# Kernel tuning notes

Hardware: AMD Instinct MI355X
Metric: run time of the kernel (lower is better)

The kernel has to match this reference:

```python
import jax, jax.numpy as jnp
import numpy as np

N_NODES = 100_000
N_EDGES = 1_250_000
IN_CH = 64
HID = 64
OUT_CH = 10
K = 5
NUM_GRAPHS = 64


def setup_inputs() -> dict:
    key = jax.random.key(0)
    ks = jax.random.split(key, 8)
    x = jax.random.normal(ks[0], (N_NODES, IN_CH), dtype=jnp.float32)
    edge_index = jax.random.randint(ks[1], (2, N_EDGES), 0, N_NODES)
    batch = jnp.sort(jax.random.randint(ks[2], (N_NODES,), 0, NUM_GRAPHS))
    s_in = float(1.0 / np.sqrt(IN_CH))
    s_h = float(1.0 / np.sqrt(HID))
    W1 = jax.random.uniform(ks[3], (K, IN_CH, HID), minval=-s_in, maxval=s_in, dtype=jnp.float32)
    b1 = jnp.zeros((HID,), jnp.float32)
    W2 = jax.random.uniform(ks[4], (K, HID, HID), minval=-s_h, maxval=s_h, dtype=jnp.float32)
    b2 = jnp.zeros((HID,), jnp.float32)
    Wfc = jax.random.uniform(ks[5], (HID, OUT_CH), minval=-s_h, maxval=s_h, dtype=jnp.float32)
    bfc = jnp.zeros((OUT_CH,), jnp.float32)
    return dict(x=x, edge_index=edge_index, batch=batch,
                W1=W1, b1=b1, W2=W2, b2=b2, Wfc=Wfc, bfc=bfc)


def _cheb_conv(x, src, dst, W, b):
    """PyG ChebConv with normalization='rw', lambda_max=2.
    L_rw = I - D^{-1} A ; scaled L_hat = 2*L/lambda_max - I = -D^{-1}A
    (self-loop weights cancel to 0), so each hop is a weighted scatter-add."""
    n = x.shape[0]
    deg = jax.ops.segment_sum(jnp.ones((src.shape[0],), x.dtype), src, num_segments=n)
    inv_deg = jnp.where(deg > 0, 1.0 / deg, 0.0)
    ew = -inv_deg[src]  # per-edge weight of L_hat

    def prop(t):  # (L_hat t)[i] = sum_{j->i} ew * t[j]
        return jax.ops.segment_sum(ew[:, None] * t[src], dst, num_segments=n)

    Tx0 = x
    out = Tx0 @ W[0]
    Tx1 = prop(Tx0)
    out = out + Tx1 @ W[1]
    for k in range(2, W.shape[0]):
        Tx2 = 2.0 * prop(Tx1) - Tx0
        out = out + Tx2 @ W[k]
        Tx0, Tx1 = Tx1, Tx2
    return out + b


def reference(x, edge_index, batch, W1, b1, W2, b2, Wfc, bfc):
    src, dst = edge_index[0], edge_index[1]
    h = jax.nn.selu(_cheb_conv(x, src, dst, W1, b1))
    # AlphaDropout is identity at inference
    h = jax.nn.selu(_cheb_conv(h, src, dst, W2, b2))
    g = jax.ops.segment_sum(h, batch, num_segments=NUM_GRAPHS)  # global_add_pool
    return g @ Wfc + bfc
```

## Files before the change

kernel.cpp:

```cpp
#include <hip/hip_runtime.h>
#include <cstdint>

#define CH 64
#define NBLK 256
#define NBMAX 1024
#define SRCMASK 0x1FFFFu

typedef __attribute__((ext_vector_type(8))) short bf16x8;
typedef __attribute__((ext_vector_type(8))) unsigned short u16x8;
typedef __attribute__((ext_vector_type(4))) float f32x4;
typedef unsigned int uint32;
typedef unsigned char uchar;

__device__ __forceinline__ unsigned short f2bf(float x) {
  unsigned u = __float_as_uint(x);
  u += 0x7FFF + ((u >> 16) & 1);
  return (unsigned short)(u >> 16);
}
__device__ __forceinline__ float bflo(uint32 u) { return __uint_as_float(u << 16); }
__device__ __forceinline__ float bfhi(uint32 u) { return __uint_as_float(u & 0xFFFF0000u); }
__device__ __forceinline__ uint32 bfpack(float lo, float hi) {
  return ((uint32)f2bf(hi) << 16) | (uint32)f2bf(lo);
}

__global__ __launch_bounds__(256) void k_b1(const int* __restrict__ src, const int* __restrict__ dst,
                                            int* __restrict__ cntD, int* __restrict__ cntS, int E, int NB) {
  __shared__ int hD[NBMAX], hS[NBMAX];
  int t = threadIdx.x, b = blockIdx.x;
  for (int i = t; i < NBMAX; i += 256) { hD[i] = 0; hS[i] = 0; }
  __syncthreads();
  int chunk = (E + NBLK - 1) / NBLK;
  int e0 = b * chunk, e1 = min(E, e0 + chunk);
  for (int e = e0 + t; e < e1; e += 256) {
    atomicAdd(&hD[dst[e] >> 7], 1);
    atomicAdd(&hS[src[e] >> 7], 1);
  }
  __syncthreads();
  for (int i = t; i < NB; i += 256) {
    cntD[i * NBLK + b] = hD[i];
    cntS[i * NBLK + b] = hS[i];
  }
}

__global__ __launch_bounds__(256) void k_scan_local(const int* __restrict__ in, int* __restrict__ out,
                                                    int* __restrict__ bsum, int total) {
  __shared__ int s[256];
  int t = threadIdx.x;
  int base = blockIdx.x * 1024 + t * 4;
  int v0 = (base + 0 < total) ? in[base + 0] : 0;
  int v1 = (base + 1 < total) ? in[base + 1] : 0;
  int v2 = (base + 2 < total) ? in[base + 2] : 0;
  int v3 = (base + 3 < total) ? in[base + 3] : 0;
  int sum = v0 + v1 + v2 + v3;
  s[t] = sum;
  __syncthreads();
  for (int off = 1; off < 256; off <<= 1) {
    int x = (t >= off) ? s[t - off] : 0;
    __syncthreads();
    s[t] += x;
    __syncthreads();
  }
  int excl = s[t] - sum;
  if (base + 0 < total) out[base + 0] = excl;  excl += v0;
  if (base + 1 < total) out[base + 1] = excl;  excl += v1;
  if (base + 2 < total) out[base + 2] = excl;  excl += v2;
  if (base + 3 < total) out[base + 3] = excl;
  if (t == 255) bsum[blockIdx.x] = s[255];
}

__global__ __launch_bounds__(256) void k_scan_bsums(int* bsum, int nb) {
  __shared__ int s[256];
  int t = threadIdx.x;
  int v = (t < nb) ? bsum[t] : 0;
  s[t] = v;
  __syncthreads();
  for (int off = 1; off < 256; off <<= 1) {
    int x = (t >= off) ? s[t - off] : 0;
    __syncthreads();
    s[t] += x;
    __syncthreads();
  }
  if (t < nb) bsum[t] = s[t] - v;
}

__global__ __launch_bounds__(256) void k_scan_add(int* __restrict__ arr, const int* __restrict__ bsum, int total) {
  int i = blockIdx.x * 256 + threadIdx.x;
  if (i < total) arr[i] += bsum[i >> 10];
}

__global__ __launch_bounds__(256) void k_b2(const int* __restrict__ src, const int* __restrict__ dst,
                                            const int* __restrict__ cbaseD, const int* __restrict__ cbaseS,
                                            uint32* __restrict__ etmp, uchar* __restrict__ svals, int E, int NB) {
  __shared__ int curD[NBMAX], curS[NBMAX];
  int t = threadIdx.x, b = blockIdx.x;
  for (int i = t; i < NB; i += 256) {
    curD[i] = cbaseD[i * NBLK + b];
    curS[i] = cbaseS[i * NBLK + b];
  }
  __syncthreads();
  int chunk = (E + NBLK - 1) / NBLK;
  int e0 = b * chunk, e1 = min(E, e0 + chunk);
  for (int e = e0 + t; e < e1; e += 256) {
    int s = src[e], d = dst[e];
    int pd = atomicAdd(&curD[d >> 7], 1);
    etmp[pd] = ((uint32)(d & 127) << 17) | (uint32)s;
    int ps = atomicAdd(&curS[s >> 7], 1);
    svals[ps] = (uchar)(s & 127);
  }
}

__global__ __launch_bounds__(256) void k_b3_deg(const uchar* __restrict__ svals, const int* __restrict__ cbaseS,
                                                float* __restrict__ neg_inv, int n, int E, int NB) {
  __shared__ int h[128];
  int t = threadIdx.x, k = blockIdx.x;
  if (t < 128) h[t] = 0;
  __syncthreads();
  int lo = cbaseS[k * NBLK];
  int hi = (k + 1 < NB) ? cbaseS[(k + 1) * NBLK] : E;
  for (int e = lo + t; e < hi; e += 256) atomicAdd(&h[svals[e]], 1);
  __syncthreads();
  if (t < 128) {
    int node = k * 128 + t;
    if (node < n) {
      int c = h[t];
      neg_inv[node] = c > 0 ? (-1.0f / (float)c) : 0.0f;
    }
  }
}

__global__ __launch_bounds__(256) void k_b3_dst(const uint32* __restrict__ etmp, const int* __restrict__ cbaseD,
                                                const float* __restrict__ neg_inv, int2* __restrict__ erec,
                                                int* __restrict__ row_ptr, int n, int E, int NB) {
  __shared__ int h[128], sc[128], cur[128];
  int t = threadIdx.x, k = blockIdx.x;
  if (t < 128) h[t] = 0;
  __syncthreads();
  int lo = cbaseD[k * NBLK];
  int hi = (k + 1 < NB) ? cbaseD[(k + 1) * NBLK] : E;
  for (int e = lo + t; e < hi; e += 256) atomicAdd(&h[(etmp[e] >> 17) & 127], 1);
  __syncthreads();
  if (t < 128) sc[t] = h[t];
  __syncthreads();
  for (int off = 1; off < 128; off <<= 1) {
    int x = (t < 128 && t >= off) ? sc[t - off] : 0;
    __syncthreads();
    if (t < 128) sc[t] += x;
    __syncthreads();
  }
  if (t < 128) {
    int excl = sc[t] - h[t];
    cur[t] = excl;
    int node = k * 128 + t;
    if (node < n) row_ptr[node] = lo + excl;
  }
  if (k == NB - 1 && t == 0) row_ptr[n] = E;
  __syncthreads();
  for (int e = lo + t; e < hi; e += 256) {
    uint32 r = etmp[e];
    int s = (int)(r & SRCMASK);
    int pos = atomicAdd(&cur[(r >> 17) & 127], 1);
    erec[lo + pos] = make_int2(s, __float_as_int(neg_inv[s]));
  }
}

__global__ __launch_bounds__(256) void k_cast(const float* __restrict__ x, unsigned short* __restrict__ xb,
                                              int total8) {
  int i = blockIdx.x * 256 + threadIdx.x;
  if (i < total8) {
    const float4* p = (const float4*)(x + (size_t)i * 8);
    float4 v0 = p[0], v1 = p[1];
    u16x8 w;
    w[0] = f2bf(v0.x); w[1] = f2bf(v0.y); w[2] = f2bf(v0.z); w[3] = f2bf(v0.w);
    w[4] = f2bf(v1.x); w[5] = f2bf(v1.y); w[6] = f2bf(v1.z); w[7] = f2bf(v1.w);
    *(u16x8*)(xb + (size_t)i * 8) = w;
  }
}

__global__ __launch_bounds__(256) void k_prop(const int* __restrict__ row_ptr, const int2* __restrict__ erec,
                                              const uint32* __restrict__ t_in,
                                              const uint32* __restrict__ t_sub,
                                              uint32* __restrict__ t_out, int n, int mode) {
  int tid = threadIdx.x;
  int lane = tid & 63;
  int cp = lane & 31;
  int h = lane >> 5;
  int node = blockIdx.x * 8 + ((tid >> 6) << 1) + h;
  bool active = node < n;
  int beg = active ? row_ptr[node] : 0;
  int end = active ? row_ptr[node + 1] : 0;
  float a0 = 0.f, a1 = 0.f, b0 = 0.f, b1 = 0.f, c0 = 0.f, c1 = 0.f, d0 = 0.f, d1 = 0.f;
  float e0a = 0.f, e1a = 0.f, f0 = 0.f, f1 = 0.f, g0 = 0.f, g1 = 0.f, h0 = 0.f, h1 = 0.f;
  int e = beg;
  for (; e + 8 <= end; e += 8) {
    int2 q0 = erec[e + 0]; int2 q1 = erec[e + 1]; int2 q2 = erec[e + 2]; int2 q3 = erec[e + 3];
    int2 q4 = erec[e + 4]; int2 q5 = erec[e + 5]; int2 q6 = erec[e + 6]; int2 q7 = erec[e + 7];
    uint32 u0 = t_in[q0.x * 32 + cp];
    uint32 u1 = t_in[q1.x * 32 + cp];
    uint32 u2 = t_in[q2.x * 32 + cp];
    uint32 u3 = t_in[q3.x * 32 + cp];
    uint32 u4 = t_in[q4.x * 32 + cp];
    uint32 u5 = t_in[q5.x * 32 + cp];
    uint32 u6 = t_in[q6.x * 32 + cp];
    uint32 u7 = t_in[q7.x * 32 + cp];
    float w0 = __int_as_float(q0.y), w1 = __int_as_float(q1.y);
    float w2 = __int_as_float(q2.y), w3 = __int_as_float(q3.y);
    float w4 = __int_as_float(q4.y), w5 = __int_as_float(q5.y);
    float w6 = __int_as_float(q6.y), w7 = __int_as_float(q7.y);
    a0 = fmaf(w0, bflo(u0), a0);   a1 = fmaf(w0, bfhi(u0), a1);
    b0 = fmaf(w1, bflo(u1), b0);   b1 = fmaf(w1, bfhi(u1), b1);
    c0 = fmaf(w2, bflo(u2), c0);   c1 = fmaf(w2, bfhi(u2), c1);
    d0 = fmaf(w3, bflo(u3), d0);   d1 = fmaf(w3, bfhi(u3), d1);
    e0a = fmaf(w4, bflo(u4), e0a); e1a = fmaf(w4, bfhi(u4), e1a);
    f0 = fmaf(w5, bflo(u5), f0);   f1 = fmaf(w5, bfhi(u5), f1);
    g0 = fmaf(w6, bflo(u6), g0);   g1 = fmaf(w6, bfhi(u6), g1);
    h0 = fmaf(w7, bflo(u7), h0);   h1 = fmaf(w7, bfhi(u7), h1);
  }
  if (e + 4 <= end) {
    int2 q0 = erec[e + 0]; int2 q1 = erec[e + 1]; int2 q2 = erec[e + 2]; int2 q3 = erec[e + 3];
    uint32 u0 = t_in[q0.x * 32 + cp];
    uint32 u1 = t_in[q1.x * 32 + cp];
    uint32 u2 = t_in[q2.x * 32 + cp];
    uint32 u3 = t_in[q3.x * 32 + cp];
    float w0 = __int_as_float(q0.y), w1 = __int_as_float(q1.y);
    float w2 = __int_as_float(q2.y), w3 = __int_as_float(q3.y);
    a0 = fmaf(w0, bflo(u0), a0);   a1 = fmaf(w0, bfhi(u0), a1);
    b0 = fmaf(w1, bflo(u1), b0);   b1 = fmaf(w1, bfhi(u1), b1);
    c0 = fmaf(w2, bflo(u2), c0);   c1 = fmaf(w2, bfhi(u2), c1);
    d0 = fmaf(w3, bflo(u3), d0);   d1 = fmaf(w3, bfhi(u3), d1);
    e += 4;
  }
  if (e + 2 <= end) {
    int2 q0 = erec[e + 0]; int2 q1 = erec[e + 1];
    uint32 u0 = t_in[q0.x * 32 + cp];
    uint32 u1 = t_in[q1.x * 32 + cp];
    float w0 = __int_as_float(q0.y), w1 = __int_as_float(q1.y);
    a0 = fmaf(w0, bflo(u0), a0);   a1 = fmaf(w0, bfhi(u0), a1);
    b0 = fmaf(w1, bflo(u1), b0);   b1 = fmaf(w1, bfhi(u1), b1);
    e += 2;
  }
  if (e < end) {
    int2 q = erec[e];
    uint32 u = t_in[q.x * 32 + cp];
    float w = __int_as_float(q.y);
    a0 = fmaf(w, bflo(u), a0);
    a1 = fmaf(w, bfhi(u), a1);
  }
  float s0 = ((a0 + b0) + (c0 + d0)) + ((e0a + f0) + (g0 + h0));
  float s1 = ((a1 + b1) + (c1 + d1)) + ((e1a + f1) + (g1 + h1));
  if (active) {
    if (mode == 2) {
      uint32 u = t_sub[(size_t)node * 32 + cp];
      s0 = 2.0f * s0 - bflo(u);
      s1 = 2.0f * s1 - bfhi(u);
    }
    t_out[(size_t)node * 32 + cp] = bfpack(s0, s1);
  }
}

__global__ __launch_bounds__(256) void k_prepW(const float* __restrict__ W, unsigned short* __restrict__ Wt) {
  int o = blockIdx.x * 256 + threadIdx.x;
  if (o < 64 * 320) {
    int j = o / 320, k = o - j * 320;
    Wt[o] = f2bf(W[k * 64 + j]);
  }
}

__device__ __forceinline__ float selu(float v) {
  const float sc = 1.0507009873554805f, al = 1.6732632423543773f;
  return (v > 0.f) ? (sc * v) : (sc * al * (expf(v) - 1.f));
}

__global__ __launch_bounds__(256) void k_gemm5(
    const unsigned short* __restrict__ M0, const unsigned short* __restrict__ M1,
    const unsigned short* __restrict__ M2, const unsigned short* __restrict__ M3,
    const unsigned short* __restrict__ M4,
    const unsigned short* __restrict__ Wt, const float* __restrict__ bias,
    unsigned short* __restrict__ outp, int n, int nstrips) {
  __shared__ unsigned short lds[2][32 * 320];
  const int t = threadIdx.x;
  const int lane = t & 63, wave = t >> 6;
  const int g = lane >> 4, r16 = lane & 15;
  const unsigned short* mats[5] = {M0, M1, M2, M3, M4};
  const int colB = wave * 16 + r16;
  bf16x8 Bf[10];
#pragma unroll
  for (int kk = 0; kk < 10; ++kk)
    Bf[kk] = *(const bf16x8*)(Wt + colB * 320 + kk * 32 + g * 8);
  const float bv = bias[colB];
  const int srow = t >> 3, scc = t & 7;

  int strip = blockIdx.x;
  if (strip >= nstrips) return;
  int cur = 0;
  {
    int node0 = strip * 32;
#pragma unroll
    for (int m = 0; m < 5; ++m) {
      int ca = m * 8 + scc;
      u16x8 w = {};
      if (node0 + srow < n)
        w = *(const u16x8*)(mats[m] + (size_t)(node0 + srow) * CH + scc * 8);
      *(u16x8*)(&lds[0][srow * 320 + ((ca ^ (srow & 7)) << 3)]) = w;
    }
  }
  __syncthreads();
  for (; strip < nstrips; strip += gridDim.x) {
    int nxt = strip + gridDim.x;
    if (nxt < nstrips) {
      int node0 = nxt * 32;
#pragma unroll
      for (int m = 0; m < 5; ++m) {
        int ca = m * 8 + scc;
        u16x8 w = {};
        if (node0 + srow < n)
          w = *(const u16x8*)(mats[m] + (size_t)(node0 + srow) * CH + scc * 8);
        *(u16x8*)(&lds[cur ^ 1][srow * 320 + ((ca ^ (srow & 7)) << 3)]) = w;
      }
    }
    const unsigned short* L = lds[cur];
    const int rowA0 = r16, rowA1 = r16 + 16;
    f32x4 acc0 = {}, acc1 = {};
#pragma unroll
    for (int kk = 0; kk < 10; ++kk) {
      int ca = kk * 4 + g;
      bf16x8 a0 = *(const bf16x8*)(&L[rowA0 * 320 + ((ca ^ (rowA0 & 7)) << 3)]);
      bf16x8 a1 = *(const bf16x8*)(&L[rowA1 * 320 + ((ca ^ (rowA1 & 7)) << 3)]);
      acc0 = __builtin_amdgcn_mfma_f32_16x16x32_bf16(a0, Bf[kk], acc0, 0, 0, 0);
      acc1 = __builtin_amdgcn_mfma_f32_16x16x32_bf16(a1, Bf[kk], acc1, 0, 0, 0);
    }
    int node0 = strip * 32;
    const f32x4 accs[2] = {acc0, acc1};
#pragma unroll
    for (int i = 0; i < 2; ++i) {
#pragma unroll
      for (int rr = 0; rr < 4; ++rr) {
        int row = node0 + i * 16 + g * 4 + rr;
        if (row < n)
          outp[(size_t)row * CH + colB] = f2bf(selu(accs[i][rr] + bv));
      }
    }
    __syncthreads();
    cur ^= 1;
  }
}

__global__ __launch_bounds__(256) void k_gemm5_pool(
    const unsigned short* __restrict__ M0, const unsigned short* __restrict__ M1,
    const unsigned short* __restrict__ M2, const unsigned short* __restrict__ M3,
    const unsigned short* __restrict__ M4,
    const unsigned short* __restrict__ Wt, const float* __restrict__ bias,
    const int* __restrict__ batch, float* __restrict__ gout, int n, int nstrips) {
  __shared__ unsigned short lds[2][32 * 320];
  const int t = threadIdx.x;
  const int lane = t & 63, wave = t >> 6;
  const int g = lane >> 4, r16 = lane & 15;
  const unsigned short* mats[5] = {M0, M1, M2, M3, M4};
  const int colB = wave * 16 + r16;
  bf16x8 Bf[10];
#pragma unroll
  for (int kk = 0; kk < 10; ++kk)
    Bf[kk] = *(const bf16x8*)(Wt + colB * 320 + kk * 32 + g * 8);
  const float bv = bias[colB];
  const int srow = t >> 3, scc = t & 7;

  int strip = blockIdx.x;
  if (strip >= nstrips) return;
  int cur = 0;
  {
    int node0 = strip * 32;
#pragma unroll
    for (int m = 0; m < 5; ++m) {
      int ca = m * 8 + scc;
      u16x8 w = {};
      if (node0 + srow < n)
        w = *(const u16x8*)(mats[m] + (size_t)(node0 + srow) * CH + scc * 8);
      *(u16x8*)(&lds[0][srow * 320 + ((ca ^ (srow & 7)) << 3)]) = w;
    }
  }
  __syncthreads();
  for (; strip < nstrips; strip += gridDim.x) {
    int nxt = strip + gridDim.x;
    if (nxt < nstrips) {
      int node0 = nxt * 32;
#pragma unroll
      for (int m = 0; m < 5; ++m) {
        int ca = m * 8 + scc;
        u16x8 w = {};
        if (node0 + srow < n)
          w = *(const u16x8*)(mats[m] + (size_t)(node0 + srow) * CH + scc * 8);
        *(u16x8*)(&lds[cur ^ 1][srow * 320 + ((ca ^ (srow & 7)) << 3)]) = w;
      }
    }
    const unsigned short* L = lds[cur];
    const int rowA0 = r16, rowA1 = r16 + 16;
    f32x4 acc0 = {}, acc1 = {};
#pragma unroll
    for (int kk = 0; kk < 10; ++kk) {
      int ca = kk * 4 + g;
      bf16x8 a0 = *(const bf16x8*)(&L[rowA0 * 320 + ((ca ^ (rowA0 & 7)) << 3)]);
      bf16x8 a1 = *(const bf16x8*)(&L[rowA1 * 320 + ((ca ^ (rowA1 & 7)) << 3)]);
      acc0 = __builtin_amdgcn_mfma_f32_16x16x32_bf16(a0, Bf[kk], acc0, 0, 0, 0);
      acc1 = __builtin_amdgcn_mfma_f32_16x16x32_bf16(a1, Bf[kk], acc1, 0, 0, 0);
    }
    __syncthreads();
    float* S = (float*)lds[cur];
    const f32x4 accs[2] = {acc0, acc1};
#pragma unroll
    for (int i = 0; i < 2; ++i)
#pragma unroll
      for (int rr = 0; rr < 4; ++rr) {
        int row = i * 16 + g * 4 + rr;
        S[row * 65 + colB] = selu(accs[i][rr] + bv);
      }
    __syncthreads();
    int node0 = strip * 32;
    int c = t & 63, w = t >> 6;
    float curv = 0.f;
    int curg = -1;
    for (int r = 0; r < 8; ++r) {
      int row = w * 8 + r;
      int gn = node0 + row;
      if (gn >= n) break;
      int b = batch[gn];
      if (b != curg) {
        if (curg >= 0) atomicAdd(&gout[curg * CH + c], curv);
        curg = b;
        curv = 0.f;
      }
      curv += S[row * 65 + c];
    }
    if (curg >= 0) atomicAdd(&gout[curg * CH + c], curv);
    __syncthreads();
    cur ^= 1;
  }
}

__global__ __launch_bounds__(256) void k_fc(const float* __restrict__ g, const float* __restrict__ Wfc,
                                            const float* __restrict__ bfc, float* __restrict__ outp,
                                            int ng, int oc) {
  int i = blockIdx.x * 256 + threadIdx.x;
  if (i < ng * oc) {
    int gi = i / oc, o = i - gi * oc;
    float s = bfc[o];
    for (int ci = 0; ci < CH; ++ci) s += g[gi * CH + ci] * Wfc[ci * oc + o];
    outp[i] = s;
  }
}

extern "C" void kernel_launch(void* const* d_in, const int* in_sizes, int n_in,
                              void* d_out, int out_size, void* d_ws, size_t ws_size,
                              hipStream_t stream) {
  const float* x   = (const float*)d_in[0];
  const int* eidx  = (const int*)d_in[1];
  const int* batch = (const int*)d_in[2];
  const float* W1  = (const float*)d_in[3];
  const float* b1  = (const float*)d_in[4];
  const float* W2  = (const float*)d_in[5];
  const float* b2  = (const float*)d_in[6];
  const float* Wfc = (const float*)d_in[7];
  const float* bfc = (const float*)d_in[8];
  float* out = (float*)d_out;

  const int n  = in_sizes[0] / CH;
  const int E  = in_sizes[1] / 2;
  const int OC = in_sizes[8];
  const int NG = out_size / OC;
  const int NB = (n + 127) >> 7;

  const int* src = eidx;
  const int* dst = eidx + E;

  size_t off = 0;
  char* base = (char*)d_ws;
  auto alloc = [&](size_t bytes) -> void* {
    size_t cur = (off + 255) & ~(size_t)255;
    off = cur + bytes;
    return (void*)(base + cur);
  };
  const int scan_total = NB * NBLK;
  const int scan_nb    = (scan_total + 1023) / 1024;
  int*   cntD   = (int*)alloc((size_t)scan_total * 4);
  int*   cntS   = (int*)alloc((size_t)scan_total * 4);
  int*   bsumD  = (int*)alloc((size_t)scan_nb * 4);
  int*   bsumS  = (int*)alloc((size_t)scan_nb * 4);
  float* neg_inv = (float*)alloc((size_t)n * 4);
  int*   row_ptr = (int*)alloc((size_t)(n + 1) * 4);
  int2*  erec    = (int2*)alloc((size_t)E * 8);
  const size_t tb16 = (size_t)n * CH * 2;
  unsigned short* Xb = (unsigned short*)alloc(tb16);
  unsigned short* T1 = (unsigned short*)alloc(tb16);
  unsigned short* T2 = (unsigned short*)alloc(tb16);
  unsigned short* T3 = (unsigned short*)alloc(tb16);
  unsigned short* T4 = (unsigned short*)alloc(tb16);
  unsigned short* H  = (unsigned short*)alloc(tb16);
  uint32* etmp  = (uint32*)alloc((size_t)E * 4);
  uchar*  svals = (uchar*)alloc((size_t)E);
  float* g  = (float*)alloc((size_t)NG * CH * 4);
  unsigned short* Wt1 = (unsigned short*)alloc(64 * 320 * 2);
  unsigned short* Wt2 = (unsigned short*)alloc(64 * 320 * 2);
  if (off > ws_size) return;

  hipMemsetAsync(g, 0, (size_t)NG * CH * 4, stream);

  k_b1<<<NBLK, 256, 0, stream>>>(src, dst, cntD, cntS, E, NB);
  k_scan_local<<<scan_nb, 256, 0, stream>>>(cntD, cntD, bsumD, scan_total);
  k_scan_bsums<<<1, 256, 0, stream>>>(bsumD, scan_nb);
  k_scan_add<<<(scan_total + 255) / 256, 256, 0, stream>>>(cntD, bsumD, scan_total);
  k_scan_local<<<scan_nb, 256, 0, stream>>>(cntS, cntS, bsumS, scan_total);
  k_scan_bsums<<<1, 256, 0, stream>>>(bsumS, scan_nb);
  k_scan_add<<<(scan_total + 255) / 256, 256, 0, stream>>>(cntS, bsumS, scan_total);
  k_b2<<<NBLK, 256, 0, stream>>>(src, dst, cntD, cntS, etmp, svals, E, NB);
  k_b3_deg<<<NB, 256, 0, stream>>>(svals, cntS, neg_inv, n, E, NB);
  k_b3_dst<<<NB, 256, 0, stream>>>(etmp, cntD, neg_inv, erec, row_ptr, n, E, NB);

  k_prepW<<<80, 256, 0, stream>>>(W1, Wt1);
  k_prepW<<<80, 256, 0, stream>>>(W2, Wt2);
  k_cast<<<(n * CH / 8 + 255) / 256, 256, 0, stream>>>(x, Xb, n * CH / 8);

  const int pb = (n + 7) / 8;
  const int nstrips = (n + 31) / 32;
  const int gb = nstrips < 1024 ? nstrips : 1024;
  k_prop<<<pb, 256, 0, stream>>>(row_ptr, erec, (const uint32*)Xb, nullptr, (uint32*)T1, n, 1);
  k_prop<<<pb, 256, 0, stream>>>(row_ptr, erec, (const uint32*)T1, (const uint32*)Xb, (uint32*)T2, n, 2);
  k_prop<<<pb, 256, 0, stream>>>(row_ptr, erec, (const uint32*)T2, (const uint32*)T1, (uint32*)T3, n, 2);
  k_prop<<<pb, 256, 0, stream>>>(row_ptr, erec, (const uint32*)T3, (const uint32*)T2, (uint32*)T4, n, 2);
  k_gemm5<<<gb, 256, 0, stream>>>(Xb, T1, T2, T3, T4, Wt1, b1, H, n, nstrips);
  k_prop<<<pb, 256, 0, stream>>>(row_ptr, erec, (const uint32*)H,  nullptr, (uint32*)T1, n, 1);
  k_prop<<<pb, 256, 0, stream>>>(row_ptr, erec, (const uint32*)T1, (const uint32*)H,  (uint32*)T2, n, 2);
  k_prop<<<pb, 256, 0, stream>>>(row_ptr, erec, (const uint32*)T2, (const uint32*)T1, (uint32*)T3, n, 2);
  k_prop<<<pb, 256, 0, stream>>>(row_ptr, erec, (const uint32*)T3, (const uint32*)T2, (uint32*)T4, n, 2);
  k_gemm5_pool<<<gb, 256, 0, stream>>>(H, T1, T2, T3, T4, Wt2, b2, batch, g, n, nstrips);
  k_fc<<<(NG * OC + 255) / 256, 256, 0, stream>>>(g, Wfc, bfc, out, NG, OC);
}
```

Baseline: 398.7 us.

## Fold Chebyshev recurrence into weights, merge scans, vectorize edge loads

Propagation kernels now compute plain powers of L_hat, with no 2*prop - T_{k-2} step. The Chebyshev polynomial coefficients are folded into the prepared GEMM weights, so the extra read of a previous tensor per hop goes away. The two count scans are merged into one scan over a concatenated buffer, with the S offsets shifted by E. Edge records are read as 16-byte pairs after aligning to an even index. Using monomial powers in bf16 can lose precision, since coefficients up to 8 amplify rounding.

```diff
diff --git a/kernel.cpp b/kernel.cpp
--- a/kernel.cpp
+++ b/kernel.cpp
@@ -46,12 +46,14 @@
                                                     int* __restrict__ bsum, int total) {
   __shared__ int s[256];
   int t = threadIdx.x;
-  int base = blockIdx.x * 1024 + t * 4;
-  int v0 = (base + 0 < total) ? in[base + 0] : 0;
-  int v1 = (base + 1 < total) ? in[base + 1] : 0;
-  int v2 = (base + 2 < total) ? in[base + 2] : 0;
-  int v3 = (base + 3 < total) ? in[base + 3] : 0;
-  int sum = v0 + v1 + v2 + v3;
+  int base = blockIdx.x * 2048 + t * 8;
+  int v[8];
+  int sum = 0;
+#pragma unroll
+  for (int i = 0; i < 8; ++i) {
+    v[i] = (base + i < total) ? in[base + i] : 0;
+    sum += v[i];
+  }
   s[t] = sum;
   __syncthreads();
   for (int off = 1; off < 256; off <<= 1) {
@@ -61,10 +63,11 @@
     __syncthreads();
   }
   int excl = s[t] - sum;
-  if (base + 0 < total) out[base + 0] = excl;  excl += v0;
-  if (base + 1 < total) out[base + 1] = excl;  excl += v1;
-  if (base + 2 < total) out[base + 2] = excl;  excl += v2;
-  if (base + 3 < total) out[base + 3] = excl;
+#pragma unroll
+  for (int i = 0; i < 8; ++i) {
+    if (base + i < total) out[base + i] = excl;
+    excl += v[i];
+  }
   if (t == 255) bsum[blockIdx.x] = s[255];
 }
 
@@ -85,7 +88,7 @@
 
 __global__ __launch_bounds__(256) void k_scan_add(int* __restrict__ arr, const int* __restrict__ bsum, int total) {
   int i = blockIdx.x * 256 + threadIdx.x;
-  if (i < total) arr[i] += bsum[i >> 10];
+  if (i < total) arr[i] += bsum[i >> 11];
 }
 
 __global__ __launch_bounds__(256) void k_b2(const int* __restrict__ src, const int* __restrict__ dst,
@@ -95,7 +98,7 @@
   int t = threadIdx.x, b = blockIdx.x;
   for (int i = t; i < NB; i += 256) {
     curD[i] = cbaseD[i * NBLK + b];
-    curS[i] = cbaseS[i * NBLK + b];
+    curS[i] = cbaseS[i * NBLK + b] - E;
   }
   __syncthreads();
   int chunk = (E + NBLK - 1) / NBLK;
@@ -115,8 +118,8 @@
   int t = threadIdx.x, k = blockIdx.x;
   if (t < 128) h[t] = 0;
   __syncthreads();
-  int lo = cbaseS[k * NBLK];
-  int hi = (k + 1 < NB) ? cbaseS[(k + 1) * NBLK] : E;
+  int lo = cbaseS[k * NBLK] - E;
+  int hi = (k + 1 < NB) ? (cbaseS[(k + 1) * NBLK] - E) : E;
   for (int e = lo + t; e < hi; e += 256) atomicAdd(&h[svals[e]], 1);
   __syncthreads();
   if (t < 128) {
@@ -178,8 +181,7 @@
 
 __global__ __launch_bounds__(256) void k_prop(const int* __restrict__ row_ptr, const int2* __restrict__ erec,
                                               const uint32* __restrict__ t_in,
-                                              const uint32* __restrict__ t_sub,
-                                              uint32* __restrict__ t_out, int n, int mode) {
+                                              uint32* __restrict__ t_out, int n) {
   int tid = threadIdx.x;
   int lane = tid & 63;
   int cp = lane & 31;
@@ -191,21 +193,31 @@
   float a0 = 0.f, a1 = 0.f, b0 = 0.f, b1 = 0.f, c0 = 0.f, c1 = 0.f, d0 = 0.f, d1 = 0.f;
   float e0a = 0.f, e1a = 0.f, f0 = 0.f, f1 = 0.f, g0 = 0.f, g1 = 0.f, h0 = 0.f, h1 = 0.f;
   int e = beg;
+  if ((e & 1) && e < end) {
+    int2 q = erec[e];
+    uint32 u = t_in[q.x * 32 + cp];
+    float w = __int_as_float(q.y);
+    a0 = fmaf(w, bflo(u), a0);
+    a1 = fmaf(w, bfhi(u), a1);
+    ++e;
+  }
   for (; e + 8 <= end; e += 8) {
-    int2 q0 = erec[e + 0]; int2 q1 = erec[e + 1]; int2 q2 = erec[e + 2]; int2 q3 = erec[e + 3];
-    int2 q4 = erec[e + 4]; int2 q5 = erec[e + 5]; int2 q6 = erec[e + 6]; int2 q7 = erec[e + 7];
-    uint32 u0 = t_in[q0.x * 32 + cp];
-    uint32 u1 = t_in[q1.x * 32 + cp];
-    uint32 u2 = t_in[q2.x * 32 + cp];
-    uint32 u3 = t_in[q3.x * 32 + cp];
-    uint32 u4 = t_in[q4.x * 32 + cp];
-    uint32 u5 = t_in[q5.x * 32 + cp];
-    uint32 u6 = t_in[q6.x * 32 + cp];
-    uint32 u7 = t_in[q7.x * 32 + cp];
-    float w0 = __int_as_float(q0.y), w1 = __int_as_float(q1.y);
-    float w2 = __int_as_float(q2.y), w3 = __int_as_float(q3.y);
-    float w4 = __int_as_float(q4.y), w5 = __int_as_float(q5.y);
-    float w6 = __int_as_float(q6.y), w7 = __int_as_float(q7.y);
+    int4 p01 = *(const int4*)(erec + e + 0);
+    int4 p23 = *(const int4*)(erec + e + 2);
+    int4 p45 = *(const int4*)(erec + e + 4);
+    int4 p67 = *(const int4*)(erec + e + 6);
+    uint32 u0 = t_in[p01.x * 32 + cp];
+    uint32 u1 = t_in[p01.z * 32 + cp];
+    uint32 u2 = t_in[p23.x * 32 + cp];
+    uint32 u3 = t_in[p23.z * 32 + cp];
+    uint32 u4 = t_in[p45.x * 32 + cp];
+    uint32 u5 = t_in[p45.z * 32 + cp];
+    uint32 u6 = t_in[p67.x * 32 + cp];
+    uint32 u7 = t_in[p67.z * 32 + cp];
+    float w0 = __int_as_float(p01.y), w1 = __int_as_float(p01.w);
+    float w2 = __int_as_float(p23.y), w3 = __int_as_float(p23.w);
+    float w4 = __int_as_float(p45.y), w5 = __int_as_float(p45.w);
+    float w6 = __int_as_float(p67.y), w7 = __int_as_float(p67.w);
     a0 = fmaf(w0, bflo(u0), a0);   a1 = fmaf(w0, bfhi(u0), a1);
     b0 = fmaf(w1, bflo(u1), b0);   b1 = fmaf(w1, bfhi(u1), b1);
     c0 = fmaf(w2, bflo(u2), c0);   c1 = fmaf(w2, bfhi(u2), c1);
@@ -216,13 +228,14 @@
     h0 = fmaf(w7, bflo(u7), h0);   h1 = fmaf(w7, bfhi(u7), h1);
   }
   if (e + 4 <= end) {
-    int2 q0 = erec[e + 0]; int2 q1 = erec[e + 1]; int2 q2 = erec[e + 2]; int2 q3 = erec[e + 3];
-    uint32 u0 = t_in[q0.x * 32 + cp];
-    uint32 u1 = t_in[q1.x * 32 + cp];
-    uint32 u2 = t_in[q2.x * 32 + cp];
-    uint32 u3 = t_in[q3.x * 32 + cp];
-    float w0 = __int_as_float(q0.y), w1 = __int_as_float(q1.y);
-    float w2 = __int_as_float(q2.y), w3 = __int_as_float(q3.y);
+    int4 p01 = *(const int4*)(erec + e + 0);
+    int4 p23 = *(const int4*)(erec + e + 2);
+    uint32 u0 = t_in[p01.x * 32 + cp];
+    uint32 u1 = t_in[p01.z * 32 + cp];
+    uint32 u2 = t_in[p23.x * 32 + cp];
+    uint32 u3 = t_in[p23.z * 32 + cp];
+    float w0 = __int_as_float(p01.y), w1 = __int_as_float(p01.w);
+    float w2 = __int_as_float(p23.y), w3 = __int_as_float(p23.w);
     a0 = fmaf(w0, bflo(u0), a0);   a1 = fmaf(w0, bfhi(u0), a1);
     b0 = fmaf(w1, bflo(u1), b0);   b1 = fmaf(w1, bfhi(u1), b1);
     c0 = fmaf(w2, bflo(u2), c0);   c1 = fmaf(w2, bfhi(u2), c1);
@@ -230,10 +243,10 @@
     e += 4;
   }
   if (e + 2 <= end) {
-    int2 q0 = erec[e + 0]; int2 q1 = erec[e + 1];
-    uint32 u0 = t_in[q0.x * 32 + cp];
-    uint32 u1 = t_in[q1.x * 32 + cp];
-    float w0 = __int_as_float(q0.y), w1 = __int_as_float(q1.y);
+    int4 p01 = *(const int4*)(erec + e);
+    uint32 u0 = t_in[p01.x * 32 + cp];
+    uint32 u1 = t_in[p01.z * 32 + cp];
+    float w0 = __int_as_float(p01.y), w1 = __int_as_float(p01.w);
     a0 = fmaf(w0, bflo(u0), a0);   a1 = fmaf(w0, bfhi(u0), a1);
     b0 = fmaf(w1, bflo(u1), b0);   b1 = fmaf(w1, bfhi(u1), b1);
     e += 2;
@@ -247,21 +260,30 @@
   }
   float s0 = ((a0 + b0) + (c0 + d0)) + ((e0a + f0) + (g0 + h0));
   float s1 = ((a1 + b1) + (c1 + d1)) + ((e1a + f1) + (g1 + h1));
-  if (active) {
-    if (mode == 2) {
-      uint32 u = t_sub[(size_t)node * 32 + cp];
-      s0 = 2.0f * s0 - bflo(u);
-      s1 = 2.0f * s1 - bfhi(u);
-    }
-    t_out[(size_t)node * 32 + cp] = bfpack(s0, s1);
-  }
+  if (active) t_out[(size_t)node * 32 + cp] = bfpack(s0, s1);
 }
 
 __global__ __launch_bounds__(256) void k_prepW(const float* __restrict__ W, unsigned short* __restrict__ Wt) {
   int o = blockIdx.x * 256 + threadIdx.x;
   if (o < 64 * 320) {
-    int j = o / 320, k = o - j * 320;
-    Wt[o] = f2bf(W[k * 64 + j]);
+    int j = o / 320;
+    int r = o - j * 320;
+    int kk = r >> 6;
+    int i = r & 63;
+    float w0 = W[0 * 4096 + i * 64 + j];
+    float w1 = W[1 * 4096 + i * 64 + j];
+    float w2 = W[2 * 4096 + i * 64 + j];
+    float w3 = W[3 * 4096 + i * 64 + j];
+    float w4 = W[4 * 4096 + i * 64 + j];
+    float v;
+    switch (kk) {
+      case 0: v = w0 - w2 + w4; break;
+      case 1: v = w1 - 3.0f * w3; break;
+      case 2: v = 2.0f * w2 - 8.0f * w4; break;
+      case 3: v = 4.0f * w3; break;
+      default: v = 8.0f * w4; break;
+    }
+    Wt[o] = f2bf(v);
   }
 }
 
@@ -478,11 +500,10 @@
     return (void*)(base + cur);
   };
   const int scan_total = NB * NBLK;
-  const int scan_nb    = (scan_total + 1023) / 1024;
-  int*   cntD   = (int*)alloc((size_t)scan_total * 4);
-  int*   cntS   = (int*)alloc((size_t)scan_total * 4);
-  int*   bsumD  = (int*)alloc((size_t)scan_nb * 4);
-  int*   bsumS  = (int*)alloc((size_t)scan_nb * 4);
+  const int scan_total2 = 2 * scan_total;
+  const int scan_nb2 = (scan_total2 + 2047) / 2048;
+  int*   cnt    = (int*)alloc((size_t)scan_total2 * 4);
+  int*   bsum   = (int*)alloc((size_t)scan_nb2 * 4);
   float* neg_inv = (float*)alloc((size_t)n * 4);
   int*   row_ptr = (int*)alloc((size_t)(n + 1) * 4);
   int2*  erec    = (int2*)alloc((size_t)E * 8);
@@ -500,15 +521,15 @@
   unsigned short* Wt2 = (unsigned short*)alloc(64 * 320 * 2);
   if (off > ws_size) return;
 
+  int* cntD = cnt;
+  int* cntS = cnt + scan_total;
+
   hipMemsetAsync(g, 0, (size_t)NG * CH * 4, stream);
 
   k_b1<<<NBLK, 256, 0, stream>>>(src, dst, cntD, cntS, E, NB);
-  k_scan_local<<<scan_nb, 256, 0, stream>>>(cntD, cntD, bsumD, scan_total);
-  k_scan_bsums<<<1, 256, 0, stream>>>(bsumD, scan_nb);
-  k_scan_add<<<(scan_total + 255) / 256, 256, 0, stream>>>(cntD, bsumD, scan_total);
-  k_scan_local<<<scan_nb, 256, 0, stream>>>(cntS, cntS, bsumS, scan_total);
-  k_scan_bsums<<<1, 256, 0, stream>>>(bsumS, scan_nb);
-  k_scan_add<<<(scan_total + 255) / 256, 256, 0, stream>>>(cntS, bsumS, scan_total);
+  k_scan_local<<<scan_nb2, 256, 0, stream>>>(cnt, cnt, bsum, scan_total2);
+  k_scan_bsums<<<1, 256, 0, stream>>>(bsum, scan_nb2);
+  k_scan_add<<<(scan_total2 + 255) / 256, 256, 0, stream>>>(cnt, bsum, scan_total2);
   k_b2<<<NBLK, 256, 0, stream>>>(src, dst, cntD, cntS, etmp, svals, E, NB);
   k_b3_deg<<<NB, 256, 0, stream>>>(svals, cntS, neg_inv, n, E, NB);
   k_b3_dst<<<NB, 256, 0, stream>>>(etmp, cntD, neg_inv, erec, row_ptr, n, E, NB);
@@ -520,15 +541,15 @@
   const int pb = (n + 7) / 8;
   const int nstrips = (n + 31) / 32;
   const int gb = nstrips < 1024 ? nstrips : 1024;
-  k_prop<<<pb, 256, 0, stream>>>(row_ptr, erec, (const uint32*)Xb, nullptr, (uint32*)T1, n, 1);
-  k_prop<<<pb, 256, 0, stream>>>(row_ptr, erec, (const uint32*)T1, (const uint32*)Xb, (uint32*)T2, n, 2);
-  k_prop<<<pb, 256, 0, stream>>>(row_ptr, erec, (const uint32*)T2, (const uint32*)T1, (uint32*)T3, n, 2);
-  k_prop<<<pb, 256, 0, stream>>>(row_ptr, erec, (const uint32*)T3, (const uint32*)T2, (uint32*)T4, n, 2);
+  k_prop<<<pb, 256, 0, stream>>>(row_ptr, erec, (const uint32*)Xb, (uint32*)T1, n);
+  k_prop<<<pb, 256, 0, stream>>>(row_ptr, erec, (const uint32*)T1, (uint32*)T2, n);
+  k_prop<<<pb, 256, 0, stream>>>(row_ptr, erec, (const uint32*)T2, (uint32*)T3, n);
+  k_prop<<<pb, 256, 0, stream>>>(row_ptr, erec, (const uint32*)T3, (uint32*)T4, n);
   k_gemm5<<<gb, 256, 0, stream>>>(Xb, T1, T2, T3, T4, Wt1, b1, H, n, nstrips);
-  k_prop<<<pb, 256, 0, stream>>>(row_ptr, erec, (const uint32*)H,  nullptr, (uint32*)T1, n, 1);
-  k_prop<<<pb, 256, 0, stream>>>(row_ptr, erec, (const uint32*)T1, (const uint32*)H,  (uint32*)T2, n, 2);
-  k_prop<<<pb, 256, 0, stream>>>(row_ptr, erec, (const uint32*)T2, (const uint32*)T1, (uint32*)T3, n, 2);
-  k_prop<<<pb, 256, 0, stream>>>(row_ptr, erec, (const uint32*)T3, (const uint32*)T2, (uint32*)T4, n, 2);
+  k_prop<<<pb, 256, 0, stream>>>(row_ptr, erec, (const uint32*)H,  (uint32*)T1, n);
+  k_prop<<<pb, 256, 0, stream>>>(row_ptr, erec, (const uint32*)T1, (uint32*)T2, n);
+  k_prop<<<pb, 256, 0, stream>>>(row_ptr, erec, (const uint32*)T2, (uint32*)T3, n);
+  k_prop<<<pb, 256, 0, stream>>>(row_ptr, erec, (const uint32*)T3, (uint32*)T4, n);
   k_gemm5_pool<<<gb, 256, 0, stream>>>(H, T1, T2, T3, T4, Wt2, b2, batch, g, n, nstrips);
   k_fc<<<(NG * OC + 255) / 256, 256, 0, stream>>>(g, Wfc, bfc, out, NG, OC);
 }
```

Result: no change. 400.7 us (+0.5%).
